# Kernel tuning notes

Measured on AMD Instinct MI355X. Metric: run time of the kernel, lower is better.

Reference implementation:

```python
import jax, jax.numpy as jnp
import numpy as np

NUM_HEADS = 8
WINDOW = 128  # num_previous_frames
EPS = 1e-5


def setup_inputs() -> dict:
    key = jax.random.key(0)
    ks = jax.random.split(key, 5)
    B, T, E = 8, 1024, 512
    x = jax.random.normal(ks[0], (B, T, E), dtype=jnp.float32)
    x_lengths = jax.random.randint(ks[1], (B,), 1, T + 1).astype(jnp.int32)
    gamma = jnp.ones((E,), dtype=jnp.float32)
    beta = jnp.zeros((E,), dtype=jnp.float32)
    sc_in = 1.0 / np.sqrt(E)
    w_in = jax.random.normal(ks[2], (3 * E, E), dtype=jnp.float32) * sc_in
    b_in = jnp.zeros((3 * E,), dtype=jnp.float32)
    w_out = jax.random.normal(ks[3], (E, E), dtype=jnp.float32) * sc_in
    b_out = jnp.zeros((E,), dtype=jnp.float32)
    return {"x": x, "x_lengths": x_lengths, "gamma": gamma, "beta": beta,
            "w_in": w_in, "b_in": b_in, "w_out": w_out, "b_out": b_out}


def _forward(x, gamma, beta, w_in, b_in, w_out, b_out):
    B, T, E = x.shape
    H = NUM_HEADS
    D = E // H
    # Timewise LayerNorm: normalize over channel dim per (batch, time)
    mu = jnp.mean(x, axis=-1, keepdims=True)
    var = jnp.mean(jnp.square(x - mu), axis=-1, keepdims=True)
    xn = (x - mu) * jax.lax.rsqrt(var + EPS) * gamma + beta
    # in-projection: qkv packed
    qkv = xn @ w_in.T + b_in  # [B,T,3E]
    q, k, v = jnp.split(qkv, 3, axis=-1)
    q = q.reshape(B, T, H, D)
    k = k.reshape(B, T, H, D)
    v = v.reshape(B, T, H, D)
    scale = 1.0 / np.sqrt(D)
    scores = jnp.einsum('bqhd,bkhd->bhqk', q * scale, k)  # [B,H,T,T]
    # banded causal mask: allow j in [i-WINDOW, i]
    i = jnp.arange(T)[:, None]
    j = jnp.arange(T)[None, :]
    allowed = (j <= i) & (j >= i - WINDOW)
    scores = jnp.where(allowed[None, None], scores, -jnp.inf)
    attn = jax.nn.softmax(scores, axis=-1)
    ctx = jnp.einsum('bhqk,bkhd->bqhd', attn, v).reshape(B, T, E)
    out = ctx @ w_out.T + b_out
    return out  # dropout is identity in eval mode


def reference(x, x_lengths, gamma, beta, w_in, b_in, w_out, b_out):
    del x_lengths  # unused by the original forward (no key_padding_mask passed)
    return _forward(x, gamma, beta, w_in, b_in, w_out, b_out)
```

## Files before the change

### kernel.cpp

```cpp
#include <hip/hip_runtime.h>
#include <stdint.h>

typedef __bf16 bf16;
typedef __bf16 bf16x8 __attribute__((ext_vector_type(8)));
typedef float f32x4 __attribute__((ext_vector_type(4)));

#define MFMA_16x16x32(a, b, c) __builtin_amdgcn_mfma_f32_16x16x32_bf16((a), (b), (c), 0, 0, 0)

__device__ __forceinline__ void gl_lds16(const bf16* g, bf16* l) {
    __builtin_amdgcn_global_load_lds(
        (const __attribute__((address_space(1))) void*)g,
        (__attribute__((address_space(3))) void*)l, 16, 0, 0);
}

__global__ void cvt_kernel(const float* __restrict__ src, bf16* __restrict__ dst, int n) {
    int i = blockIdx.x * blockDim.x + threadIdx.x;
    if (i < n) dst[i] = (bf16)src[i];
}

__global__ __launch_bounds__(256) void ln_kernel(const float* __restrict__ x,
                                                 const bf16* __restrict__ gamma,
                                                 const bf16* __restrict__ beta,
                                                 bf16* __restrict__ xn) {
    const int lane = threadIdx.x & 63;
    const int row = (blockIdx.x << 2) + (threadIdx.x >> 6);
    const size_t base = (size_t)row * 512 + lane * 8;
    const float* xf = x + base;
    float4 a = *(const float4*)xf;
    float4 b = *(const float4*)(xf + 4);
    float f[8] = {a.x, a.y, a.z, a.w, b.x, b.y, b.z, b.w};
    float s = 0.f;
#pragma unroll
    for (int j = 0; j < 8; ++j) s += f[j];
#pragma unroll
    for (int off = 32; off >= 1; off >>= 1) s += __shfl_xor(s, off, 64);
    const float mu = s * (1.0f / 512.0f);
    float vs = 0.f;
#pragma unroll
    for (int j = 0; j < 8; ++j) { float d = f[j] - mu; vs += d * d; }
#pragma unroll
    for (int off = 32; off >= 1; off >>= 1) vs += __shfl_xor(vs, off, 64);
    const float rstd = rsqrtf(vs * (1.0f / 512.0f) + 1e-5f);
    bf16x8 g = *(const bf16x8*)(gamma + lane * 8);
    bf16x8 bb = *(const bf16x8*)(beta + lane * 8);
    bf16x8 o;
#pragma unroll
    for (int j = 0; j < 8; ++j)
        o[j] = (bf16)((f[j] - mu) * rstd * (float)g[j] + (float)bb[j]);
    *(bf16x8*)(xn + base) = o;
}

template <typename OT>
__global__ __launch_bounds__(256) void gemm_bt(const bf16* __restrict__ A,
                                               const bf16* __restrict__ B,
                                               const bf16* __restrict__ bias,
                                               OT* __restrict__ C,
                                               int N, int K) {
    __shared__ alignas(16) bf16 As[128 * 32];
    __shared__ alignas(16) bf16 Bs[128 * 32];
    const int tid = threadIdx.x;
    const int lane = tid & 63;
    const int wid = tid >> 6;
    const int wm = (wid >> 1) * 64, wn = (wid & 1) * 64;
    const int m0 = blockIdx.y * 128, n0 = blockIdx.x * 128;
    const int l15 = lane & 15, l16 = lane >> 4;

    f32x4 acc[4][4] = {};

    const int c0 = tid, c1 = 256 + tid;
    const int ra0 = c0 >> 2, ka0 = (c0 & 3) * 8;
    const int ra1 = c1 >> 2, ka1 = (c1 & 3) * 8;
    const bf16* Abase = A + (size_t)m0 * K;
    const bf16* Bbase = B + (size_t)n0 * K;

    for (int k0 = 0; k0 < K; k0 += 32) {
        gl_lds16(Abase + (size_t)ra0 * K + k0 + ka0, &As[c0 * 8]);
        gl_lds16(Abase + (size_t)ra1 * K + k0 + ka1, &As[c1 * 8]);
        gl_lds16(Bbase + (size_t)ra0 * K + k0 + ka0, &Bs[c0 * 8]);
        gl_lds16(Bbase + (size_t)ra1 * K + k0 + ka1, &Bs[c1 * 8]);
        __syncthreads();
        bf16x8 af[4], bfr[4];
#pragma unroll
        for (int t = 0; t < 4; ++t) {
            af[t]  = *(const bf16x8*)&As[(wm + t * 16 + l15) * 32 + l16 * 8];
            bfr[t] = *(const bf16x8*)&Bs[(wn + t * 16 + l15) * 32 + l16 * 8];
        }
#pragma unroll
        for (int i = 0; i < 4; ++i)
#pragma unroll
            for (int j = 0; j < 4; ++j)
                acc[i][j] = MFMA_16x16x32(af[i], bfr[j], acc[i][j]);
        __syncthreads();
    }

#pragma unroll
    for (int j = 0; j < 4; ++j) {
        const int col = n0 + wn + j * 16 + l15;
        const float bv = (float)bias[col];
#pragma unroll
        for (int i = 0; i < 4; ++i) {
            const int rbase = m0 + wm + i * 16 + l16 * 4;
#pragma unroll
            for (int r = 0; r < 4; ++r)
                C[(size_t)(rbase + r) * N + col] = (OT)(acc[i][j][r] + bv);
        }
    }
}

#define KS_STRIDE 72
#define VS_STRIDE 200
#define PW_STRIDE 40

__global__ __launch_bounds__(256) void attn_kernel(const bf16* __restrict__ qkv,
                                                   bf16* __restrict__ ctx) {
    __shared__ alignas(16) bf16 Ks[192 * KS_STRIDE];
    __shared__ alignas(16) bf16 Vs[64 * VS_STRIDE];
    __shared__ alignas(16) bf16 Pbuf[4 * 16 * PW_STRIDE];

    const int tid = threadIdx.x;
    const int lane = tid & 63, wid = tid >> 6;
    const int l15 = lane & 15, l16 = lane >> 4;
    const int bh = blockIdx.y, b = bh >> 3, h = bh & 7;
    const int q0 = blockIdx.x * 64;
    const int kv0 = (q0 > 128) ? (q0 - 128) : 0;
    const int nk = q0 + 64 - kv0;
    const size_t tokbase = (size_t)b * 1024;

    for (int c = tid; c < nk * 8; c += 256) {
        const int kk = c >> 3, dc = (c & 7) * 8;
        const bf16* src = qkv + (tokbase + kv0 + kk) * 1536 + h * 64 + dc;
        uint4 kw = *(const uint4*)(src + 512);
        *(uint4*)&Ks[kk * KS_STRIDE + dc] = kw;
        uint4 vw = *(const uint4*)(src + 1024);
        const bf16* vp = (const bf16*)&vw;
#pragma unroll
        for (int j = 0; j < 8; ++j) Vs[(dc + j) * VS_STRIDE + kk] = vp[j];
    }

    const int qt0 = q0 + wid * 16;
    const bf16* qptr = qkv + (tokbase + qt0 + l15) * 1536 + h * 64;
    bf16x8 qa0 = *(const bf16x8*)(qptr + l16 * 8);
    bf16x8 qa1 = *(const bf16x8*)(qptr + 32 + l16 * 8);

    __syncthreads();

    bf16* Pw = &Pbuf[wid * 16 * PW_STRIDE];
    f32x4 of[4] = {};
    float mst[4], lst[4];
#pragma unroll
    for (int r = 0; r < 4; ++r) { mst[r] = -1e30f; lst[r] = 0.f; }

    const int ktstart = ((qt0 > 128) ? (qt0 - 128) : 0) & ~31;
    for (int kt = ktstart; kt <= qt0 + 15; kt += 32) {
        const int krel = kt - kv0;
        f32x4 s0 = {}, s1 = {};
        {
            const bf16* kb0 = &Ks[(krel + l15) * KS_STRIDE + l16 * 8];
            const bf16* kb1 = kb0 + 16 * KS_STRIDE;
            s0 = MFMA_16x16x32(qa0, *(const bf16x8*)kb0, s0);
            s0 = MFMA_16x16x32(qa1, *(const bf16x8*)(kb0 + 32), s0);
            s1 = MFMA_16x16x32(qa0, *(const bf16x8*)kb1, s1);
            s1 = MFMA_16x16x32(qa1, *(const bf16x8*)(kb1 + 32), s1);
        }
        float e0[4], e1[4];
#pragma unroll
        for (int r = 0; r < 4; ++r) {
            const int qa = qt0 + l16 * 4 + r;
            const int kg0 = kt + l15;
            const int kg1 = kg0 + 16;
            const bool ok0 = (kg0 <= qa) && (kg0 >= qa - 128);
            const bool ok1 = (kg1 <= qa) && (kg1 >= qa - 128);
            float v0 = ok0 ? s0[r] * 0.125f : -1e30f;
            float v1 = ok1 ? s1[r] * 0.125f : -1e30f;
            float mx = fmaxf(v0, v1);
#pragma unroll
            for (int off = 1; off < 16; off <<= 1)
                mx = fmaxf(mx, __shfl_xor(mx, off, 64));
            const float mnew = fmaxf(mst[r], mx);
            const float alpha = __expf(mst[r] - mnew);
            e0[r] = ok0 ? __expf(v0 - mnew) : 0.f;
            e1[r] = ok1 ? __expf(v1 - mnew) : 0.f;
            float rs = e0[r] + e1[r];
#pragma unroll
            for (int off = 1; off < 16; off <<= 1)
                rs += __shfl_xor(rs, off, 64);
            lst[r] = lst[r] * alpha + rs;
            mst[r] = mnew;
#pragma unroll
            for (int nt = 0; nt < 4; ++nt) of[nt][r] *= alpha;
        }
#pragma unroll
        for (int r = 0; r < 4; ++r) {
            const int q = l16 * 4 + r;
            Pw[q * PW_STRIDE + l15] = (bf16)e0[r];
            Pw[q * PW_STRIDE + 16 + l15] = (bf16)e1[r];
        }
        __asm__ volatile("s_waitcnt lgkmcnt(0)" ::: "memory");
        bf16x8 pa = *(const bf16x8*)&Pw[l15 * PW_STRIDE + l16 * 8];
#pragma unroll
        for (int nt = 0; nt < 4; ++nt) {
            const bf16* vb = &Vs[(nt * 16 + l15) * VS_STRIDE + krel + l16 * 8];
            of[nt] = MFMA_16x16x32(pa, *(const bf16x8*)vb, of[nt]);
        }
        __asm__ volatile("s_waitcnt lgkmcnt(0)" ::: "memory");
    }

    float linv[4];
#pragma unroll
    for (int r = 0; r < 4; ++r) linv[r] = 1.0f / lst[r];
    bf16* cbase = ctx + (tokbase + qt0) * 512 + h * 64;
#pragma unroll
    for (int nt = 0; nt < 4; ++nt)
#pragma unroll
        for (int r = 0; r < 4; ++r) {
            const int q = l16 * 4 + r;
            cbase[(size_t)q * 512 + nt * 16 + l15] = (bf16)(of[nt][r] * linv[r]);
        }
}

extern "C" void kernel_launch(void* const* d_in, const int* in_sizes, int n_in,
                              void* d_out, int out_size, void* d_ws, size_t ws_size,
                              hipStream_t stream) {
    const float* x     = (const float*)d_in[0];
    const float* gamma = (const float*)d_in[2];
    const float* beta  = (const float*)d_in[3];
    const float* w_in  = (const float*)d_in[4];
    const float* b_in  = (const float*)d_in[5];
    const float* w_out = (const float*)d_in[6];
    const float* b_out = (const float*)d_in[7];
    float* out = (float*)d_out;

    char* ws = (char*)d_ws;
    bf16* cw_in  = (bf16*)ws;
    bf16* cw_out = cw_in + 786432;
    bf16* cb_in  = cw_out + 262144;
    bf16* cb_out = cb_in + 1536;
    bf16* cgam   = cb_out + 512;
    bf16* cbet   = cgam + 512;
    bf16* xn     = (bf16*)(ws + (4u << 20));
    bf16* qkv    = (bf16*)(ws + (12u << 20));
    bf16* ctx    = xn;

    cvt_kernel<<<3072, 256, 0, stream>>>(w_in,  cw_in,  786432);
    cvt_kernel<<<1024, 256, 0, stream>>>(w_out, cw_out, 262144);
    cvt_kernel<<<6,    256, 0, stream>>>(b_in,  cb_in,  1536);
    cvt_kernel<<<2,    256, 0, stream>>>(b_out, cb_out, 512);
    cvt_kernel<<<2,    256, 0, stream>>>(gamma, cgam,   512);
    cvt_kernel<<<2,    256, 0, stream>>>(beta,  cbet,   512);

    ln_kernel<<<2048, 256, 0, stream>>>(x, cgam, cbet, xn);
    gemm_bt<bf16><<<dim3(12, 64), 256, 0, stream>>>(xn, cw_in, cb_in, qkv, 1536, 512);
    attn_kernel<<<dim3(16, 64), 256, 0, stream>>>(qkv, ctx);
    gemm_bt<float><<<dim3(4, 64), 256, 0, stream>>>(ctx, cw_out, cb_out, out, 512, 512);
}
```

Before: 156.1 us.

## Fuse prep kernels, use fp32 params directly, retile out-proj, row-major V in attention

Merges the six conversion launches and the LayerNorm kernel into a single prep kernel that converts weights with vectorized loads, and reads gamma, beta and biases directly as fp32. The GEMM is templated on M tile size so the output projection uses 64-row tiles, doubling its block count for better CU occupancy. Attention now stores V row-major, which avoids the scalar transposed LDS stores, but in exchange the PV step gathers eight scalar LDS reads per fragment with clamped row indices. Together these cut launch overhead and conversion traffic, at the risk of slower V fragment loads.

```diff
diff --git a/kernel.cpp b/kernel.cpp
--- a/kernel.cpp
+++ b/kernel.cpp
@@ -13,80 +13,101 @@
         (__attribute__((address_space(3))) void*)l, 16, 0, 0);
 }
 
-__global__ void cvt_kernel(const float* __restrict__ src, bf16* __restrict__ dst, int n) {
-    int i = blockIdx.x * blockDim.x + threadIdx.x;
-    if (i < n) dst[i] = (bf16)src[i];
-}
-
-__global__ __launch_bounds__(256) void ln_kernel(const float* __restrict__ x,
-                                                 const bf16* __restrict__ gamma,
-                                                 const bf16* __restrict__ beta,
-                                                 bf16* __restrict__ xn) {
-    const int lane = threadIdx.x & 63;
-    const int row = (blockIdx.x << 2) + (threadIdx.x >> 6);
-    const size_t base = (size_t)row * 512 + lane * 8;
-    const float* xf = x + base;
-    float4 a = *(const float4*)xf;
-    float4 b = *(const float4*)(xf + 4);
-    float f[8] = {a.x, a.y, a.z, a.w, b.x, b.y, b.z, b.w};
-    float s = 0.f;
-#pragma unroll
-    for (int j = 0; j < 8; ++j) s += f[j];
-#pragma unroll
-    for (int off = 32; off >= 1; off >>= 1) s += __shfl_xor(s, off, 64);
-    const float mu = s * (1.0f / 512.0f);
-    float vs = 0.f;
-#pragma unroll
-    for (int j = 0; j < 8; ++j) { float d = f[j] - mu; vs += d * d; }
-#pragma unroll
-    for (int off = 32; off >= 1; off >>= 1) vs += __shfl_xor(vs, off, 64);
-    const float rstd = rsqrtf(vs * (1.0f / 512.0f) + 1e-5f);
-    bf16x8 g = *(const bf16x8*)(gamma + lane * 8);
-    bf16x8 bb = *(const bf16x8*)(beta + lane * 8);
-    bf16x8 o;
-#pragma unroll
-    for (int j = 0; j < 8; ++j)
-        o[j] = (bf16)((f[j] - mu) * rstd * (float)g[j] + (float)bb[j]);
-    *(bf16x8*)(xn + base) = o;
-}
-
-template <typename OT>
+__global__ __launch_bounds__(256) void prep_kernel(const float* __restrict__ x,
+                                                   const float* __restrict__ gamma,
+                                                   const float* __restrict__ beta,
+                                                   const float* __restrict__ w_in,
+                                                   const float* __restrict__ w_out,
+                                                   bf16* __restrict__ xn,
+                                                   bf16* __restrict__ cw_in,
+                                                   bf16* __restrict__ cw_out) {
+    const int bid = blockIdx.x;
+    if (bid < 2048) {
+        const int lane = threadIdx.x & 63;
+        const int row = (bid << 2) + (threadIdx.x >> 6);
+        const size_t base = (size_t)row * 512 + lane * 8;
+        const float* xf = x + base;
+        float4 a = *(const float4*)xf;
+        float4 b = *(const float4*)(xf + 4);
+        float f[8] = {a.x, a.y, a.z, a.w, b.x, b.y, b.z, b.w};
+        float s = 0.f;
+#pragma unroll
+        for (int j = 0; j < 8; ++j) s += f[j];
+#pragma unroll
+        for (int off = 32; off >= 1; off >>= 1) s += __shfl_xor(s, off, 64);
+        const float mu = s * (1.0f / 512.0f);
+        float vs = 0.f;
+#pragma unroll
+        for (int j = 0; j < 8; ++j) { float d = f[j] - mu; vs += d * d; }
+#pragma unroll
+        for (int off = 32; off >= 1; off >>= 1) vs += __shfl_xor(vs, off, 64);
+        const float rstd = rsqrtf(vs * (1.0f / 512.0f) + 1e-5f);
+        float4 g0 = *(const float4*)(gamma + lane * 8);
+        float4 g1 = *(const float4*)(gamma + lane * 8 + 4);
+        float4 b0 = *(const float4*)(beta + lane * 8);
+        float4 b1 = *(const float4*)(beta + lane * 8 + 4);
+        float gg[8] = {g0.x, g0.y, g0.z, g0.w, g1.x, g1.y, g1.z, g1.w};
+        float bb[8] = {b0.x, b0.y, b0.z, b0.w, b1.x, b1.y, b1.z, b1.w};
+        bf16x8 o;
+#pragma unroll
+        for (int j = 0; j < 8; ++j)
+            o[j] = (bf16)((f[j] - mu) * rstd * gg[j] + bb[j]);
+        *(bf16x8*)(xn + base) = o;
+    } else {
+        const float* src;
+        bf16* dst;
+        int base;
+        if (bid < 2432) { src = w_in;  dst = cw_in;  base = (bid - 2048) * 2048; }
+        else            { src = w_out; dst = cw_out; base = (bid - 2432) * 2048; }
+        const int i = base + threadIdx.x * 8;
+        float4 a = *(const float4*)(src + i);
+        float4 b = *(const float4*)(src + i + 4);
+        float f[8] = {a.x, a.y, a.z, a.w, b.x, b.y, b.z, b.w};
+        bf16x8 o;
+#pragma unroll
+        for (int j = 0; j < 8; ++j) o[j] = (bf16)f[j];
+        *(bf16x8*)(dst + i) = o;
+    }
+}
+
+template <int TM, typename OT>
 __global__ __launch_bounds__(256) void gemm_bt(const bf16* __restrict__ A,
                                                const bf16* __restrict__ B,
-                                               const bf16* __restrict__ bias,
+                                               const float* __restrict__ bias,
                                                OT* __restrict__ C,
                                                int N, int K) {
-    __shared__ alignas(16) bf16 As[128 * 32];
+    constexpr int MI = TM / 32;
+    __shared__ alignas(16) bf16 As[TM * 32];
     __shared__ alignas(16) bf16 Bs[128 * 32];
     const int tid = threadIdx.x;
     const int lane = tid & 63;
     const int wid = tid >> 6;
-    const int wm = (wid >> 1) * 64, wn = (wid & 1) * 64;
-    const int m0 = blockIdx.y * 128, n0 = blockIdx.x * 128;
+    const int wm = (wid >> 1) * (TM / 2), wn = (wid & 1) * 64;
+    const int m0 = blockIdx.y * TM, n0 = blockIdx.x * 128;
     const int l15 = lane & 15, l16 = lane >> 4;
 
-    f32x4 acc[4][4] = {};
-
-    const int c0 = tid, c1 = 256 + tid;
-    const int ra0 = c0 >> 2, ka0 = (c0 & 3) * 8;
-    const int ra1 = c1 >> 2, ka1 = (c1 & 3) * 8;
+    f32x4 acc[MI][4] = {};
+
     const bf16* Abase = A + (size_t)m0 * K;
     const bf16* Bbase = B + (size_t)n0 * K;
 
     for (int k0 = 0; k0 < K; k0 += 32) {
-        gl_lds16(Abase + (size_t)ra0 * K + k0 + ka0, &As[c0 * 8]);
-        gl_lds16(Abase + (size_t)ra1 * K + k0 + ka1, &As[c1 * 8]);
-        gl_lds16(Bbase + (size_t)ra0 * K + k0 + ka0, &Bs[c0 * 8]);
-        gl_lds16(Bbase + (size_t)ra1 * K + k0 + ka1, &Bs[c1 * 8]);
+#pragma unroll
+        for (int c = tid; c < TM * 4; c += 256)
+            gl_lds16(Abase + (size_t)(c >> 2) * K + k0 + (c & 3) * 8, &As[c * 8]);
+#pragma unroll
+        for (int c = tid; c < 512; c += 256)
+            gl_lds16(Bbase + (size_t)(c >> 2) * K + k0 + (c & 3) * 8, &Bs[c * 8]);
         __syncthreads();
-        bf16x8 af[4], bfr[4];
-#pragma unroll
-        for (int t = 0; t < 4; ++t) {
-            af[t]  = *(const bf16x8*)&As[(wm + t * 16 + l15) * 32 + l16 * 8];
+        bf16x8 af[MI], bfr[4];
+#pragma unroll
+        for (int t = 0; t < MI; ++t)
+            af[t] = *(const bf16x8*)&As[(wm + t * 16 + l15) * 32 + l16 * 8];
+#pragma unroll
+        for (int t = 0; t < 4; ++t)
             bfr[t] = *(const bf16x8*)&Bs[(wn + t * 16 + l15) * 32 + l16 * 8];
-        }
-#pragma unroll
-        for (int i = 0; i < 4; ++i)
+#pragma unroll
+        for (int i = 0; i < MI; ++i)
 #pragma unroll
             for (int j = 0; j < 4; ++j)
                 acc[i][j] = MFMA_16x16x32(af[i], bfr[j], acc[i][j]);
@@ -96,9 +117,9 @@
 #pragma unroll
     for (int j = 0; j < 4; ++j) {
         const int col = n0 + wn + j * 16 + l15;
-        const float bv = (float)bias[col];
-#pragma unroll
-        for (int i = 0; i < 4; ++i) {
+        const float bv = bias[col];
+#pragma unroll
+        for (int i = 0; i < MI; ++i) {
             const int rbase = m0 + wm + i * 16 + l16 * 4;
 #pragma unroll
             for (int r = 0; r < 4; ++r)
@@ -108,13 +129,13 @@
 }
 
 #define KS_STRIDE 72
-#define VS_STRIDE 200
+#define VN_STRIDE 74
 #define PW_STRIDE 40
 
 __global__ __launch_bounds__(256) void attn_kernel(const bf16* __restrict__ qkv,
                                                    bf16* __restrict__ ctx) {
     __shared__ alignas(16) bf16 Ks[192 * KS_STRIDE];
-    __shared__ alignas(16) bf16 Vs[64 * VS_STRIDE];
+    __shared__ alignas(16) bf16 Vn[192 * VN_STRIDE];
     __shared__ alignas(16) bf16 Pbuf[4 * 16 * PW_STRIDE];
 
     const int tid = threadIdx.x;
@@ -132,9 +153,8 @@
         uint4 kw = *(const uint4*)(src + 512);
         *(uint4*)&Ks[kk * KS_STRIDE + dc] = kw;
         uint4 vw = *(const uint4*)(src + 1024);
-        const bf16* vp = (const bf16*)&vw;
-#pragma unroll
-        for (int j = 0; j < 8; ++j) Vs[(dc + j) * VS_STRIDE + kk] = vp[j];
+        uint* vdst = (uint*)&Vn[kk * VN_STRIDE + dc];
+        vdst[0] = vw.x; vdst[1] = vw.y; vdst[2] = vw.z; vdst[3] = vw.w;
     }
 
     const int qt0 = q0 + wid * 16;
@@ -197,10 +217,19 @@
         }
         __asm__ volatile("s_waitcnt lgkmcnt(0)" ::: "memory");
         bf16x8 pa = *(const bf16x8*)&Pw[l15 * PW_STRIDE + l16 * 8];
+        int row[8];
+#pragma unroll
+        for (int j = 0; j < 8; ++j) {
+            int rr = krel + l16 * 8 + j;
+            row[j] = (rr < nk) ? rr : (nk - 1);
+        }
 #pragma unroll
         for (int nt = 0; nt < 4; ++nt) {
-            const bf16* vb = &Vs[(nt * 16 + l15) * VS_STRIDE + krel + l16 * 8];
-            of[nt] = MFMA_16x16x32(pa, *(const bf16x8*)vb, of[nt]);
+            bf16x8 vb;
+#pragma unroll
+            for (int j = 0; j < 8; ++j)
+                vb[j] = Vn[row[j] * VN_STRIDE + nt * 16 + l15];
+            of[nt] = MFMA_16x16x32(pa, vb, of[nt]);
         }
         __asm__ volatile("s_waitcnt lgkmcnt(0)" ::: "memory");
     }
@@ -233,23 +262,12 @@
     char* ws = (char*)d_ws;
     bf16* cw_in  = (bf16*)ws;
     bf16* cw_out = cw_in + 786432;
-    bf16* cb_in  = cw_out + 262144;
-    bf16* cb_out = cb_in + 1536;
-    bf16* cgam   = cb_out + 512;
-    bf16* cbet   = cgam + 512;
     bf16* xn     = (bf16*)(ws + (4u << 20));
     bf16* qkv    = (bf16*)(ws + (12u << 20));
     bf16* ctx    = xn;
 
-    cvt_kernel<<<3072, 256, 0, stream>>>(w_in,  cw_in,  786432);
-    cvt_kernel<<<1024, 256, 0, stream>>>(w_out, cw_out, 262144);
-    cvt_kernel<<<6,    256, 0, stream>>>(b_in,  cb_in,  1536);
-    cvt_kernel<<<2,    256, 0, stream>>>(b_out, cb_out, 512);
-    cvt_kernel<<<2,    256, 0, stream>>>(gamma, cgam,   512);
-    cvt_kernel<<<2,    256, 0, stream>>>(beta,  cbet,   512);
-
-    ln_kernel<<<2048, 256, 0, stream>>>(x, cgam, cbet, xn);
-    gemm_bt<bf16><<<dim3(12, 64), 256, 0, stream>>>(xn, cw_in, cb_in, qkv, 1536, 512);
+    prep_kernel<<<2560, 256, 0, stream>>>(x, gamma, beta, w_in, w_out, xn, cw_in, cw_out);
+    gemm_bt<128, bf16><<<dim3(12, 64), 256, 0, stream>>>(xn, cw_in, b_in, qkv, 1536, 512);
     attn_kernel<<<dim3(16, 64), 256, 0, stream>>>(qkv, ctx);
-    gemm_bt<float><<<dim3(4, 64), 256, 0, stream>>>(ctx, cw_out, cb_out, out, 512, 512);
-}
+    gemm_bt<64, float><<<dim3(4, 128), 256, 0, stream>>>(ctx, cw_out, b_out, out, 512, 512);
+}
```

Result: faster. 142.4 us (-8.8%).
